# Optimization experiments

Measured on AMD Instinct MI355X. Metric: run time of the kernel, lower is better.

## Reference

```python
import jax, jax.numpy as jnp
import numpy as np
from jax import lax

B, T, D, V = 64, 2048, 256, 256

def setup_inputs() -> dict:
    key = jax.random.key(0)
    k0, k1, k2, k3, k4 = jax.random.split(key, 5)
    s = 1.0 / np.sqrt(D)
    return {
        "tokens": jax.random.randint(k0, (B, T), 0, V),
        "E": jax.random.normal(k1, (V, D), dtype=jnp.float32) * s,
        "Wx_w": jax.random.normal(k2, (D, D), dtype=jnp.float32) * s,
        "Wh_w": jax.random.normal(k3, (D, D), dtype=jnp.float32) * s,
        "Wz_w": jax.random.normal(k4, (D, D), dtype=jnp.float32) * s,
    }

def reference(tokens, E, Wx_w, Wh_w, Wz_w):
    x = E[tokens]                              # [B,T,D] embedding lookup
    Wx = jnp.einsum('btd,ed->bte', x, Wx_w)    # precomputed input projection
    gate = jax.nn.sigmoid(jnp.einsum('btd,ed->bte', x, Wz_w))  # sigmoid(W_z x_t)
    h0 = jnp.zeros((B, D), dtype=x.dtype)

    def step(h, inp):
        wx_t, g_t = inp                        # [B,D] each
        h = jnp.tanh(wx_t + h @ Wh_w.T)        # Elman recurrence
        return h, h * g_t

    _, ys = lax.scan(step, h0, (jnp.swapaxes(Wx, 0, 1), jnp.swapaxes(gate, 0, 1)))
    out = jnp.swapaxes(ys, 0, 1)               # [B,T,D]
    return jnp.einsum('btd,vd->btv', out, E)   # tied head: logits [B,T,V]
```

## Files before the change

### kernel.cpp

```cpp
#include <hip/hip_runtime.h>

typedef _Float16 half2v __attribute__((ext_vector_type(2)));
typedef _Float16 half8 __attribute__((ext_vector_type(8)));
typedef float floatx4 __attribute__((ext_vector_type(4)));

#define T_LEN 2048

#define LDS_BARRIER() asm volatile("s_waitcnt lgkmcnt(0)\n\ts_barrier" ::: "memory")

#if __has_builtin(__builtin_amdgcn_fdot2)
#define FDOT2(a, b, c) __builtin_amdgcn_fdot2((a), (b), (c), false)
#else
static __device__ inline float fdot2_fallback(half2v a, half2v b, float c) {
    return fmaf((float)a[1], (float)b[1], fmaf((float)a[0], (float)b[0], c));
}
#define FDOT2(a, b, c) fdot2_fallback((a), (b), (c))
#endif

__global__ __launch_bounds__(256) void precompute_k(
    const float* __restrict__ E, const float* __restrict__ Wx,
    const float* __restrict__ Wh, const float* __restrict__ Wz,
    float2* __restrict__ wgt, _Float16* __restrict__ Whf)
{
    const int v = blockIdx.x, e = threadIdx.x;
    __shared__ float Ev[256];
    Ev[e] = E[v * 256 + e];
    __syncthreads();
    float ax = 0.f, az = 0.f;
    #pragma unroll 4
    for (int d = 0; d < 256; d += 4) {
        float4 ev = *(const float4*)&Ev[d];
        float4 wx = *(const float4*)&Wx[e * 256 + d];
        float4 wz = *(const float4*)&Wz[e * 256 + d];
        ax += ev.x * wx.x + ev.y * wx.y + ev.z * wx.z + ev.w * wx.w;
        az += ev.x * wz.x + ev.y * wz.y + ev.z * wz.z + ev.w * wz.w;
    }
    float2 o; o.x = ax; o.y = 1.f / (1.f + __expf(-az));
    wgt[v * 256 + e] = o;
    Whf[v * 256 + e] = (_Float16)Wh[v * 256 + e];
}

__global__ __launch_bounds__(256, 1) void rnn_k(
    const int* __restrict__ tokens, const float2* __restrict__ wgt,
    const _Float16* __restrict__ Whf, float* __restrict__ y)
{
    const int tid = threadIdx.x;
    const int w   = tid >> 6;
    const int l   = tid & 63;
    const int g   = l & 15, kq = l >> 4;
    const int b   = blockIdx.x;
    const int dbase = (w << 6) + (g << 2);
    const int k0    = kq << 6;
    const int dout  = dbase + kq;

#define WHV(j, c) wh_##j##_##c
#define DECL_WH(j, c)                                                          \
    half8 WHV(j, c) = *(const half8*)(Whf + (dbase + (j)) * 256 + k0 + ((c) << 3)); \
    asm volatile("" : "+v"(WHV(j, c)));
#define DECL_WH_ROW(j) \
    DECL_WH(j,0) DECL_WH(j,1) DECL_WH(j,2) DECL_WH(j,3) \
    DECL_WH(j,4) DECL_WH(j,5) DECL_WH(j,6) DECL_WH(j,7)
    DECL_WH_ROW(0) DECL_WH_ROW(1) DECL_WH_ROW(2) DECL_WH_ROW(3)

    __shared__ __align__(16) _Float16 hb[2][4][72];
    __shared__ unsigned char tokL[T_LEN];

    for (int i = tid; i < T_LEN; i += 256)
        tokL[i] = (unsigned char)tokens[b * T_LEN + i];
    for (int i = tid; i < 2 * 4 * 72; i += 256) ((_Float16*)hb)[i] = (_Float16)0.f;
    LDS_BARRIER();

    unsigned int yoff = (unsigned)(b * (T_LEN * 256) + dout) * 4u;

    float wx_e, g_e, wx_o, g_o;
    {
        const int t0 = tokL[0], t1 = tokL[1];
        float2 a = wgt[t0 * 256 + dout]; wx_e = a.x; g_e = a.y;
        float2 c = wgt[t1 * 256 + dout]; wx_o = c.x; g_o = c.y;
    }

#define DOT_PAIR(c, I0, I1)                                                    \
        {                                                                      \
            half2v hp = __builtin_shufflevector(hv, hv, I0, I1);               \
            ac0 = FDOT2(__builtin_shufflevector(WHV(0,c), WHV(0,c), I0, I1), hp, ac0); \
            ac1 = FDOT2(__builtin_shufflevector(WHV(1,c), WHV(1,c), I0, I1), hp, ac1); \
            ac2 = FDOT2(__builtin_shufflevector(WHV(2,c), WHV(2,c), I0, I1), hp, ac2); \
            ac3 = FDOT2(__builtin_shufflevector(WHV(3,c), WHV(3,c), I0, I1), hp, ac3); \
        }

#define DOT_C(CUR, c)                                                          \
        {                                                                      \
            half8 hv = *(const half8*)&hb[CUR][kq][(c) << 3];                  \
            DOT_PAIR(c, 0, 1) DOT_PAIR(c, 2, 3)                                \
            DOT_PAIR(c, 4, 5) DOT_PAIR(c, 6, 7)                                \
        }

#define STEP(tcur, CUR, NXT, WX, G)                                            \
    {                                                                          \
        int tf = (tcur) + 2; if (tf > T_LEN - 1) tf = T_LEN - 1;               \
        const int tok = tokL[tf];                                              \
        float ac0 = 0.f, ac1 = 0.f, ac2 = 0.f, ac3 = 0.f;                      \
        DOT_C(CUR, 0) DOT_C(CUR, 1) DOT_C(CUR, 2) DOT_C(CUR, 3)                \
        DOT_C(CUR, 4) DOT_C(CUR, 5) DOT_C(CUR, 6) DOT_C(CUR, 7)                \
        ac0 += __shfl_xor(ac0, 16); ac0 += __shfl_xor(ac0, 32);                \
        ac1 += __shfl_xor(ac1, 16); ac1 += __shfl_xor(ac1, 32);                \
        ac2 += __shfl_xor(ac2, 16); ac2 += __shfl_xor(ac2, 32);                \
        ac3 += __shfl_xor(ac3, 16); ac3 += __shfl_xor(ac3, 32);                \
        float s01 = (kq & 1) ? ac1 : ac0;                                      \
        float s23 = (kq & 1) ? ac3 : ac2;                                      \
        float sv  = (kq & 2) ? s23 : s01;                                      \
        float pre = sv + WX;                                                   \
        float ex  = __builtin_amdgcn_exp2f(pre * 2.885390082f);                \
        float hval = fmaf(__builtin_amdgcn_rcpf(ex + 1.f), -2.f, 1.f);         \
        __builtin_nontemporal_store(hval * G, (float*)((char*)y + yoff));      \
        yoff += 1024;                                                          \
        hb[NXT][w][(g << 2) + kq] = (_Float16)hval;                            \
        { const float2* gp = wgt + tok * 256 + dout; float2 a = *gp;           \
          WX = a.x; G = a.y; }                                                 \
        LDS_BARRIER();                                                         \
    }

    for (int t = 0; t < T_LEN; t += 2) {
        STEP(t,     0, 1, wx_e, g_e)
        STEP(t + 1, 1, 0, wx_o, g_o)
    }
#undef STEP
#undef DOT_C
#undef DOT_PAIR
#undef DECL_WH_ROW
#undef DECL_WH
#undef WHV
}

__device__ inline half8 cvt8(const float* p) {
    float4 u = *(const float4*)p;
    float4 w = *(const float4*)(p + 4);
    half8 r;
    r[0] = (_Float16)u.x; r[1] = (_Float16)u.y; r[2] = (_Float16)u.z; r[3] = (_Float16)u.w;
    r[4] = (_Float16)w.x; r[5] = (_Float16)w.y; r[6] = (_Float16)w.z; r[7] = (_Float16)w.w;
    return r;
}

__global__ __launch_bounds__(256) void logits_k(
    const float* __restrict__ E, float* __restrict__ io)
{
    const int tid = threadIdx.x;
    const int wv = tid >> 6;
    const int l  = tid & 63;
    const int n  = l & 15, q = l >> 4;
    const int rowbase = blockIdx.x << 6;
    const int k0base = q << 3;

    floatx4 acc[4][4];
    #pragma unroll
    for (int mt = 0; mt < 4; ++mt)
        #pragma unroll
        for (int tn = 0; tn < 4; ++tn) acc[mt][tn] = 0.f;

    #pragma unroll
    for (int ks = 0; ks < 8; ++ks) {
        const int k0 = (ks << 5) + k0base;
        half8 a[4], bfr[4];
        #pragma unroll
        for (int mt = 0; mt < 4; ++mt)
            a[mt] = cvt8(io + (rowbase + (mt << 4) + n) * 256 + k0);
        #pragma unroll
        for (int tn = 0; tn < 4; ++tn)
            bfr[tn] = cvt8(E + ((wv << 6) + (tn << 4) + n) * 256 + k0);
        #pragma unroll
        for (int mt = 0; mt < 4; ++mt)
            #pragma unroll
            for (int tn = 0; tn < 4; ++tn)
                acc[mt][tn] = __builtin_amdgcn_mfma_f32_16x16x32_f16(a[mt], bfr[tn], acc[mt][tn], 0, 0, 0);
    }
    __syncthreads();
    #pragma unroll
    for (int mt = 0; mt < 4; ++mt)
        #pragma unroll
        for (int tn = 0; tn < 4; ++tn)
            #pragma unroll
            for (int r = 0; r < 4; ++r)
                io[(rowbase + (mt << 4) + (q << 2) + r) * 256 + (wv << 6) + (tn << 4) + n] = acc[mt][tn][r];
}

extern "C" void kernel_launch(void* const* d_in, const int* in_sizes, int n_in,
                              void* d_out, int out_size, void* d_ws, size_t ws_size,
                              hipStream_t stream) {
    const int*   tokens = (const int*)d_in[0];
    const float* E      = (const float*)d_in[1];
    const float* Wx     = (const float*)d_in[2];
    const float* Wh     = (const float*)d_in[3];
    const float* Wz     = (const float*)d_in[4];
    float* out = (float*)d_out;

    char* ws = (char*)d_ws;
    float2*   wgt = (float2*)ws;
    _Float16* Whf = (_Float16*)(ws + (512 << 10));

    precompute_k<<<256, 256, 0, stream>>>(E, Wx, Wh, Wz, wgt, Whf);
    rnn_k<<<64, 256, 0, stream>>>(tokens, wgt, Whf, out);
    logits_k<<<2048, 256, 0, stream>>>(E, out);
}
```

Baseline: 1.402 ms.

## Process two batch rows per RNN block sharing register-resident Wh

Each RNN block now runs two independent batch sequences with the same register-held fp16 Wh slices, so each weight register feeds two dot products and one barrier per step covers both sequences. The grid is halved from 64 to 32 blocks. The aim is to hide the latency of the serial recurrence (LDS reads, shuffles, barrier) by interleaving two independent chains. The cost is twice the arithmetic per step on each block and half as many CUs in use, which could lengthen the critical path if the step is compute-bound rather than latency-bound.

```diff
diff --git a/kernel.cpp b/kernel.cpp
--- a/kernel.cpp
+++ b/kernel.cpp
@@ -48,7 +48,7 @@
     const int w   = tid >> 6;
     const int l   = tid & 63;
     const int g   = l & 15, kq = l >> 4;
-    const int b   = blockIdx.x;
+    const int b0  = blockIdx.x << 1;
     const int dbase = (w << 6) + (g << 2);
     const int k0    = kq << 6;
     const int dout  = dbase + kq;
@@ -62,69 +62,88 @@
     DECL_WH(j,4) DECL_WH(j,5) DECL_WH(j,6) DECL_WH(j,7)
     DECL_WH_ROW(0) DECL_WH_ROW(1) DECL_WH_ROW(2) DECL_WH_ROW(3)
 
-    __shared__ __align__(16) _Float16 hb[2][4][72];
-    __shared__ unsigned char tokL[T_LEN];
-
-    for (int i = tid; i < T_LEN; i += 256)
-        tokL[i] = (unsigned char)tokens[b * T_LEN + i];
-    for (int i = tid; i < 2 * 4 * 72; i += 256) ((_Float16*)hb)[i] = (_Float16)0.f;
+    __shared__ __align__(16) _Float16 hb[2][2][4][72];
+    __shared__ unsigned char tokL[2][T_LEN];
+
+    for (int i = tid; i < 2 * T_LEN; i += 256) {
+        const int hh = i >> 11, t = i & (T_LEN - 1);
+        tokL[hh][t] = (unsigned char)tokens[(b0 + hh) * T_LEN + t];
+    }
+    for (int i = tid; i < 2 * 2 * 4 * 72; i += 256) ((_Float16*)hb)[i] = (_Float16)0.f;
     LDS_BARRIER();
 
-    unsigned int yoff = (unsigned)(b * (T_LEN * 256) + dout) * 4u;
-
-    float wx_e, g_e, wx_o, g_o;
+    unsigned int yoffA = (unsigned)(b0 * (T_LEN * 256) + dout) * 4u;
+    unsigned int yoffB = (unsigned)((b0 + 1) * (T_LEN * 256) + dout) * 4u;
+
+    float wxAe, gAe, wxAo, gAo, wxBe, gBe, wxBo, gBo;
     {
-        const int t0 = tokL[0], t1 = tokL[1];
-        float2 a = wgt[t0 * 256 + dout]; wx_e = a.x; g_e = a.y;
-        float2 c = wgt[t1 * 256 + dout]; wx_o = c.x; g_o = c.y;
+        float2 a = wgt[tokL[0][0] * 256 + dout]; wxAe = a.x; gAe = a.y;
+        float2 c = wgt[tokL[0][1] * 256 + dout]; wxAo = c.x; gAo = c.y;
+        float2 d = wgt[tokL[1][0] * 256 + dout]; wxBe = d.x; gBe = d.y;
+        float2 e = wgt[tokL[1][1] * 256 + dout]; wxBo = e.x; gBo = e.y;
     }
 
 #define DOT_PAIR(c, I0, I1)                                                    \
         {                                                                      \
-            half2v hp = __builtin_shufflevector(hv, hv, I0, I1);               \
-            ac0 = FDOT2(__builtin_shufflevector(WHV(0,c), WHV(0,c), I0, I1), hp, ac0); \
-            ac1 = FDOT2(__builtin_shufflevector(WHV(1,c), WHV(1,c), I0, I1), hp, ac1); \
-            ac2 = FDOT2(__builtin_shufflevector(WHV(2,c), WHV(2,c), I0, I1), hp, ac2); \
-            ac3 = FDOT2(__builtin_shufflevector(WHV(3,c), WHV(3,c), I0, I1), hp, ac3); \
+            half2v hA = __builtin_shufflevector(hvA, hvA, I0, I1);             \
+            half2v hB = __builtin_shufflevector(hvB, hvB, I0, I1);             \
+            half2v w0 = __builtin_shufflevector(WHV(0,c), WHV(0,c), I0, I1);   \
+            half2v w1 = __builtin_shufflevector(WHV(1,c), WHV(1,c), I0, I1);   \
+            half2v w2 = __builtin_shufflevector(WHV(2,c), WHV(2,c), I0, I1);   \
+            half2v w3 = __builtin_shufflevector(WHV(3,c), WHV(3,c), I0, I1);   \
+            ac0 = FDOT2(w0, hA, ac0); bc0 = FDOT2(w0, hB, bc0);                \
+            ac1 = FDOT2(w1, hA, ac1); bc1 = FDOT2(w1, hB, bc1);                \
+            ac2 = FDOT2(w2, hA, ac2); bc2 = FDOT2(w2, hB, bc2);                \
+            ac3 = FDOT2(w3, hA, ac3); bc3 = FDOT2(w3, hB, bc3);                \
         }
 
 #define DOT_C(CUR, c)                                                          \
         {                                                                      \
-            half8 hv = *(const half8*)&hb[CUR][kq][(c) << 3];                  \
+            half8 hvA = *(const half8*)&hb[0][CUR][kq][(c) << 3];              \
+            half8 hvB = *(const half8*)&hb[1][CUR][kq][(c) << 3];              \
             DOT_PAIR(c, 0, 1) DOT_PAIR(c, 2, 3)                                \
             DOT_PAIR(c, 4, 5) DOT_PAIR(c, 6, 7)                                \
         }
 
-#define STEP(tcur, CUR, NXT, WX, G)                                            \
+#define FINISH(c0, c1, c2, c3, NXT, WX, G, YOFF, BI, tok)                      \
     {                                                                          \
-        int tf = (tcur) + 2; if (tf > T_LEN - 1) tf = T_LEN - 1;               \
-        const int tok = tokL[tf];                                              \
-        float ac0 = 0.f, ac1 = 0.f, ac2 = 0.f, ac3 = 0.f;                      \
-        DOT_C(CUR, 0) DOT_C(CUR, 1) DOT_C(CUR, 2) DOT_C(CUR, 3)                \
-        DOT_C(CUR, 4) DOT_C(CUR, 5) DOT_C(CUR, 6) DOT_C(CUR, 7)                \
-        ac0 += __shfl_xor(ac0, 16); ac0 += __shfl_xor(ac0, 32);                \
-        ac1 += __shfl_xor(ac1, 16); ac1 += __shfl_xor(ac1, 32);                \
-        ac2 += __shfl_xor(ac2, 16); ac2 += __shfl_xor(ac2, 32);                \
-        ac3 += __shfl_xor(ac3, 16); ac3 += __shfl_xor(ac3, 32);                \
-        float s01 = (kq & 1) ? ac1 : ac0;                                      \
-        float s23 = (kq & 1) ? ac3 : ac2;                                      \
+        c0 += __shfl_xor(c0, 16); c0 += __shfl_xor(c0, 32);                    \
+        c1 += __shfl_xor(c1, 16); c1 += __shfl_xor(c1, 32);                    \
+        c2 += __shfl_xor(c2, 16); c2 += __shfl_xor(c2, 32);                    \
+        c3 += __shfl_xor(c3, 16); c3 += __shfl_xor(c3, 32);                    \
+        float s01 = (kq & 1) ? c1 : c0;                                        \
+        float s23 = (kq & 1) ? c3 : c2;                                        \
         float sv  = (kq & 2) ? s23 : s01;                                      \
         float pre = sv + WX;                                                   \
         float ex  = __builtin_amdgcn_exp2f(pre * 2.885390082f);                \
         float hval = fmaf(__builtin_amdgcn_rcpf(ex + 1.f), -2.f, 1.f);         \
-        __builtin_nontemporal_store(hval * G, (float*)((char*)y + yoff));      \
-        yoff += 1024;                                                          \
-        hb[NXT][w][(g << 2) + kq] = (_Float16)hval;                            \
-        { const float2* gp = wgt + tok * 256 + dout; float2 a = *gp;           \
+        __builtin_nontemporal_store(hval * G, (float*)((char*)y + YOFF));      \
+        YOFF += 1024;                                                          \
+        hb[BI][NXT][w][(g << 2) + kq] = (_Float16)hval;                        \
+        { const float2* gp = wgt + (tok) * 256 + dout; float2 a = *gp;         \
           WX = a.x; G = a.y; }                                                 \
+    }
+
+#define STEP(tcur, CUR, NXT, WXA, GA, WXB, GB)                                 \
+    {                                                                          \
+        int tf = (tcur) + 2; if (tf > T_LEN - 1) tf = T_LEN - 1;               \
+        const int tokA = tokL[0][tf];                                          \
+        const int tokB = tokL[1][tf];                                          \
+        float ac0 = 0.f, ac1 = 0.f, ac2 = 0.f, ac3 = 0.f;                      \
+        float bc0 = 0.f, bc1 = 0.f, bc2 = 0.f, bc3 = 0.f;                      \
+        DOT_C(CUR, 0) DOT_C(CUR, 1) DOT_C(CUR, 2) DOT_C(CUR, 3)                \
+        DOT_C(CUR, 4) DOT_C(CUR, 5) DOT_C(CUR, 6) DOT_C(CUR, 7)                \
+        FINISH(ac0, ac1, ac2, ac3, NXT, WXA, GA, yoffA, 0, tokA)               \
+        FINISH(bc0, bc1, bc2, bc3, NXT, WXB, GB, yoffB, 1, tokB)               \
         LDS_BARRIER();                                                         \
     }
 
     for (int t = 0; t < T_LEN; t += 2) {
-        STEP(t,     0, 1, wx_e, g_e)
-        STEP(t + 1, 1, 0, wx_o, g_o)
+        STEP(t,     0, 1, wxAe, gAe, wxBe, gBe)
+        STEP(t + 1, 1, 0, wxAo, gAo, wxBo, gBo)
     }
 #undef STEP
+#undef FINISH
 #undef DOT_C
 #undef DOT_PAIR
 #undef DECL_WH_ROW
@@ -198,6 +217,6 @@
     _Float16* Whf = (_Float16*)(ws + (512 << 10));
 
     precompute_k<<<256, 256, 0, stream>>>(E, Wx, Wh, Wz, wgt, Whf);
-    rnn_k<<<64, 256, 0, stream>>>(tokens, wgt, Whf, out);
+    rnn_k<<<32, 256, 0, stream>>>(tokens, wgt, Whf, out);
     logits_k<<<2048, 256, 0, stream>>>(E, out);
 }
```

After: 2.562 ms. 82.7% more time.
